# Kernel optimization log

Hardware: AMD Instinct MI355X
Metric: run time of the kernel (lower is better)

The kernel has to match this reference:

```python
import jax, jax.numpy as jnp
import numpy as np

D_MODEL = 96
N_HEAD = 3
HEAD_DIM = D_MODEL // N_HEAD  # 32
D_FF = 2048
WIDTH = 65
HALF_W = (WIDTH - 1) // 2  # 32
EPS = 1e-5


def layer_norm(x, g, b):
    mu = jnp.mean(x, axis=-1, keepdims=True)
    var = jnp.mean(jnp.square(x - mu), axis=-1, keepdims=True)
    return (x - mu) * jax.lax.rsqrt(var + EPS) * g + b


def setup_inputs() -> dict:
    key = jax.random.key(0)
    ks = jax.random.split(key, 8)
    B, T = 8, 2048
    s = 0.05
    return {
        "x": jax.random.normal(ks[0], (B, D_MODEL, T), dtype=jnp.float32),
        "w_qkv": jax.random.normal(ks[1], (3 * D_MODEL, D_MODEL), dtype=jnp.float32) * s,
        "b_qkv": jnp.zeros((3 * D_MODEL,), dtype=jnp.float32),
        "w_out": jax.random.normal(ks[2], (D_MODEL, D_MODEL), dtype=jnp.float32) * s,
        "b_out": jnp.zeros((D_MODEL,), dtype=jnp.float32),
        "ln1_g": jnp.ones((D_MODEL,), dtype=jnp.float32),
        "ln1_b": jnp.zeros((D_MODEL,), dtype=jnp.float32),
        "w_ff1": jax.random.normal(ks[3], (D_FF, D_MODEL), dtype=jnp.float32) * s,
        "b_ff1": jnp.zeros((D_FF,), dtype=jnp.float32),
        "w_ff2": jax.random.normal(ks[4], (D_MODEL, D_FF), dtype=jnp.float32) * s,
        "b_ff2": jnp.zeros((D_MODEL,), dtype=jnp.float32),
        "ln2_g": jnp.ones((D_MODEL,), dtype=jnp.float32),
        "ln2_b": jnp.zeros((D_MODEL,), dtype=jnp.float32),
        "lnf_g": jnp.ones((D_MODEL,), dtype=jnp.float32),
        "lnf_b": jnp.zeros((D_MODEL,), dtype=jnp.float32),
    }


def reference(x, w_qkv, b_qkv, w_out, b_out, ln1_g, ln1_b, w_ff1, b_ff1,
              w_ff2, b_ff2, ln2_g, ln2_b, lnf_g, lnf_b):
    # x: (B, C, T) -> (B, T, C)
    h = jnp.transpose(x, (0, 2, 1))
    B, T, C = h.shape

    # --- multi-head self-attention with banded mask ---
    qkv = h @ w_qkv.T + b_qkv                      # (B, T, 3C)
    q, k, v = jnp.split(qkv, 3, axis=-1)
    q = q.reshape(B, T, N_HEAD, HEAD_DIM)
    k = k.reshape(B, T, N_HEAD, HEAD_DIM)
    v = v.reshape(B, T, N_HEAD, HEAD_DIM)

    scale = 1.0 / jnp.sqrt(jnp.float32(HEAD_DIM))
    scores = jnp.einsum("bthd,bshd->bhts", q, k) * scale  # (B, H, T, T)

    idx = jnp.arange(T)
    band = jnp.abs(idx[:, None] - idx[None, :]) <= HALF_W  # |i-j| <= half width
    scores = jnp.where(band[None, None], scores, jnp.float32(-jnp.inf))

    attn = jax.nn.softmax(scores, axis=-1)
    ctx = jnp.einsum("bhts,bshd->bthd", attn, v).reshape(B, T, C)
    attn_out = ctx @ w_out.T + b_out

    # --- post-norm encoder layer (dropout inactive / eval mode) ---
    h = layer_norm(h + attn_out, ln1_g, ln1_b)
    ff = jax.nn.relu(h @ w_ff1.T + b_ff1) @ w_ff2.T + b_ff2
    h = layer_norm(h + ff, ln2_g, ln2_b)

    # extra layernorm applied when width is not None
    h = layer_norm(h, lnf_g, lnf_b)

    # (B, T, C) -> (B, C, T)
    return jnp.transpose(h, (0, 2, 1))
```

## Files before the change

### kernel.cpp

```cpp
#include <hip/hip_runtime.h>
#include <hip/hip_bf16.h>

#define B 8
#define T 2048
#define C 96
#define NH 3
#define HD 32
#define FFD 2048
#define HALF_W 32
#define BT (B*T)

typedef __hip_bfloat16 bf16;
typedef __attribute__((ext_vector_type(8))) short short8;
typedef __attribute__((ext_vector_type(4))) short short4v;
typedef __attribute__((ext_vector_type(16))) float floatx16;

__device__ __forceinline__ short f2bs(float v){
    __hip_bfloat16 h = __float2bfloat16(v);
    return *reinterpret_cast<short*>(&h);
}
__device__ __forceinline__ float bs2f(short s){
    unsigned u = ((unsigned)(unsigned short)s) << 16;
    return __uint_as_float(u);
}
__device__ __forceinline__ short8 ld_b64x2(const short* p){
    short4v a = *(const short4v*)p;
    short4v b = *(const short4v*)(p + 4);
    short8 v;
    v[0]=a[0]; v[1]=a[1]; v[2]=a[2]; v[3]=a[3];
    v[4]=b[0]; v[5]=b[1]; v[6]=b[2]; v[7]=b[3];
    return v;
}
__device__ __forceinline__ int4 exch_pair(int a0,int a1,int b0,int b1,int hq){
    int ra0=__shfl_xor(a0,32), ra1=__shfl_xor(a1,32);
    int rb0=__shfl_xor(b0,32), rb1=__shfl_xor(b1,32);
    int4 s;
    s.x = hq ? rb0 : a0;
    s.y = hq ? rb1 : a1;
    s.z = hq ? b0  : ra0;
    s.w = hq ? b1  : ra1;
    return s;
}
__device__ __forceinline__ void proj_pack(const floatx16& acc, const float* bias32, int hq,
                                          short8& f0, short8& f1){
    int pkq[4][2];
    #pragma unroll
    for(int q = 0; q < 4; ++q){
        float4 bv = *(const float4*)(bias32 + 8*q + 4*hq);
        short4v t;
        t[0]=f2bs(acc[4*q+0]+bv.x); t[1]=f2bs(acc[4*q+1]+bv.y);
        t[2]=f2bs(acc[4*q+2]+bv.z); t[3]=f2bs(acc[4*q+3]+bv.w);
        int2 u = *(int2*)&t; pkq[q][0]=u.x; pkq[q][1]=u.y;
    }
    int4 r0 = exch_pair(pkq[0][0],pkq[0][1],pkq[1][0],pkq[1][1],hq);
    int4 r1 = exch_pair(pkq[2][0],pkq[2][1],pkq[3][0],pkq[3][1],hq);
    f0 = *(short8*)&r0; f1 = *(short8*)&r1;
}

__global__ void cvtw_kernel(const float* __restrict__ wq, const float* __restrict__ wo,
                            const float* __restrict__ w1, const float* __restrict__ w2,
                            bf16* __restrict__ dst){
    int i = blockIdx.x*256 + threadIdx.x;
    if(i < 27648){
        int e = i&7, lane = (i>>3)&63, r = i>>9;
        int ks = r%6, ot = r/6;
        int o = ot*32 + (lane&31);
        int k = ks*16 + (lane>>5)*8 + e;
        dst[i] = __float2bfloat16(wq[o*96 + k]);
    } else if(i < 36864){
        int j = i - 27648;
        int e = j&7, lane = (j>>3)&63, r = j>>9;
        int ks = r%6, ct = r/6;
        int c = ct*32 + (lane&31);
        int k = ks*16 + (lane>>5)*8 + e;
        dst[i] = __float2bfloat16(wo[c*96 + k]);
    } else if(i < 233472){
        int j = i - 36864;
        int e = j&7, lane = (j>>3)&63, r = j>>9;
        int ks = r%6; r /= 6;
        int w = r%4, jt = r/4;
        int row = jt*128 + w*32 + (lane&31);
        int k = ks*16 + (lane>>5)*8 + e;
        dst[i] = __float2bfloat16(w1[row*96 + k]);
    } else if(i < 430080){
        int j = i - 233472;
        int e = j&7, lane = (j>>3)&63, r = j>>9;
        int ct = r%3; r /= 3;
        int g = r%2; r /= 2;
        int w = r%4, jt = r/4;
        int c = ct*32 + (lane&31);
        int k = jt*128 + w*32 + g*16 + (lane>>5)*8 + e;
        dst[i] = __float2bfloat16(w2[c*FFD + k]);
    }
}

__global__ __launch_bounds__(384, 4) void attn_kernel(
    const float* __restrict__ x,
    const bf16* __restrict__ wqs, const bf16* __restrict__ wos,
    const float* __restrict__ b_qkv, const float* __restrict__ b_out,
    const float* __restrict__ g1, const float* __restrict__ bb1,
    bf16* __restrict__ h1b){
    __shared__ __align__(16) char smem[45952];
    short* XS   = (short*)smem;
    short* PTS  = (short*)smem;
    short* VTS  = (short*)(smem + 19200);
    short* CTX  = (short*)(smem + 38400);
    float* LSS  = (float*)(smem + 44800);
    float* RED1 = (float*)(smem + 45184);

    const int tid = threadIdx.x;
    const int u = tid >> 6, lane = tid & 63;
    const int lm = lane & 31, hq = lane >> 5;
    const int grp = u / 3, h = u % 3;
    const int b  = blockIdx.x & 7;
    const int tt = blockIdx.x >> 3;
    const int t0 = tt * 32;
    const float* xb = x + (size_t)b*C*T;

    int tg0 = t0 - 32;
    if(tg0 >= 0 && t0 + 64 <= T){
        for(int e = tid; e < 96*24; e += 384){
            int c = e / 24, t4 = e % 24;
            float4 v = *(const float4*)(xb + (size_t)c*T + tg0 + t4*4);
            XS[(t4*4+0)*100 + c] = f2bs(v.x);
            XS[(t4*4+1)*100 + c] = f2bs(v.y);
            XS[(t4*4+2)*100 + c] = f2bs(v.z);
            XS[(t4*4+3)*100 + c] = f2bs(v.w);
        }
    } else {
        for(int e = tid; e < 96*96; e += 384){
            int c = e / 96, j = e % 96;
            int t = tg0 + j; t = t < 0 ? 0 : (t > T-1 ? T-1 : t);
            XS[j*100 + c] = f2bs(xb[(size_t)c*T + t]);
        }
    }
    __syncthreads();

    short8 wof[6];
    if(u < 3){
        #pragma unroll
        for(int ks = 0; ks < 6; ++ks)
            wof[ks] = *(const short8*)((const short*)wos + (size_t)(u*6 + ks)*512 + lane*8);
    }

    short8 kf[3][2], qf0, qf1;
    if(grp == 0){
        short8 kwf[6];
        #pragma unroll
        for(int ks = 0; ks < 6; ++ks)
            kwf[ks] = *(const short8*)((const short*)wqs + (size_t)((3+h)*6 + ks)*512 + lane*8);
        #pragma unroll
        for(int tau = 0; tau < 3; ++tau){
            short8 bfr[6];
            #pragma unroll
            for(int ks = 0; ks < 6; ++ks)
                bfr[ks] = *(const short8*)(XS + (tau*32+lm)*100 + ks*16 + hq*8);
            floatx16 acc;
            #pragma unroll
            for(int r = 0; r < 16; ++r) acc[r] = 0.f;
            #pragma unroll
            for(int ks = 0; ks < 6; ++ks)
                acc = __builtin_amdgcn_mfma_f32_32x32x16_bf16(kwf[ks], bfr[ks], acc, 0,0,0);
            proj_pack(acc, b_qkv + (3+h)*32, hq, kf[tau][0], kf[tau][1]);
            if(tau == 1){
                floatx16 qa;
                #pragma unroll
                for(int r = 0; r < 16; ++r) qa[r] = 0.f;
                #pragma unroll
                for(int ks = 0; ks < 6; ++ks){
                    short8 qwf = *(const short8*)((const short*)wqs + (size_t)(h*6 + ks)*512 + lane*8);
                    qa = __builtin_amdgcn_mfma_f32_32x32x16_bf16(qwf, bfr[ks], qa, 0,0,0);
                }
                proj_pack(qa, b_qkv + h*32, hq, qf0, qf1);
            }
        }
    } else {
        short8 vwf[6];
        #pragma unroll
        for(int ks = 0; ks < 6; ++ks)
            vwf[ks] = *(const short8*)((const short*)wqs + (size_t)((6+h)*6 + ks)*512 + lane*8);
        #pragma unroll
        for(int tau = 0; tau < 3; ++tau){
            short8 bfr[6];
            #pragma unroll
            for(int ks = 0; ks < 6; ++ks)
                bfr[ks] = *(const short8*)(XS + (tau*32+lm)*100 + ks*16 + hq*8);
            floatx16 acc;
            #pragma unroll
            for(int r = 0; r < 16; ++r) acc[r] = 0.f;
            #pragma unroll
            for(int ks = 0; ks < 6; ++ks)
                acc = __builtin_amdgcn_mfma_f32_32x32x16_bf16(vwf[ks], bfr[ks], acc, 0,0,0);
            #pragma unroll
            for(int q = 0; q < 4; ++q){
                float4 bv = *(const float4*)(b_qkv + (6+h)*32 + 8*q + 4*hq);
                float bva[4] = {bv.x, bv.y, bv.z, bv.w};
                #pragma unroll
                for(int r = 0; r < 4; ++r)
                    VTS[h*3200 + (8*q + 4*hq + r)*100 + tau*32 + lm] = f2bs(acc[4*q+r] + bva[r]);
            }
        }
    }
    __syncthreads();

    if(grp == 0){
        floatx16 S[3];
        #pragma unroll
        for(int sub = 0; sub < 3; ++sub){
            floatx16 z;
            #pragma unroll
            for(int r = 0; r < 16; ++r) z[r] = 0.f;
            z = __builtin_amdgcn_mfma_f32_32x32x16_bf16(kf[sub][0], qf0, z, 0,0,0);
            z = __builtin_amdgcn_mfma_f32_32x32x16_bf16(kf[sub][1], qf1, z, 0,0,0);
            S[sub] = z;
        }
        const float scale = 0.17677669529663687f;
        float part = 0.f;
        #pragma unroll
        for(int sub = 0; sub < 3; ++sub){
            #pragma unroll
            for(int r = 0; r < 16; ++r){
                int key_local = sub*32 + (r&3) + 8*(r>>2) + 4*hq;
                int s_glob = t0 - 32 + key_local;
                int rel = key_local - lm;
                bool ok = (rel >= 0) && (rel <= 64) && (s_glob >= 0) && (s_glob < T);
                float pe = ok ? __expf(S[sub][r]*scale) : 0.f;
                S[sub][r] = pe;
                part += pe;
            }
        }
        float ltot = part + __shfl_xor(part, 32);
        if(hq == 0) LSS[h*32 + lm] = ltot;
        #pragma unroll
        for(int sub = 0; sub < 3; ++sub){
            #pragma unroll
            for(int q4 = 0; q4 < 4; ++q4){
                int kbase = sub*32 + 8*q4 + 4*hq;
                short4v pk4;
                pk4[0] = f2bs(S[sub][4*q4+0]);
                pk4[1] = f2bs(S[sub][4*q4+1]);
                pk4[2] = f2bs(S[sub][4*q4+2]);
                pk4[3] = f2bs(S[sub][4*q4+3]);
                *(short4v*)(PTS + h*3200 + lm*100 + kbase) = pk4;
            }
        }
        floatx16 O;
        #pragma unroll
        for(int r = 0; r < 16; ++r) O[r] = 0.f;
        #pragma unroll
        for(int ks = 0; ks < 6; ++ks){
            short8 pa = ld_b64x2(PTS + h*3200 + lm*100 + ks*16 + hq*8);
            short8 vf = ld_b64x2(VTS + h*3200 + lm*100 + ks*16 + hq*8);
            O = __builtin_amdgcn_mfma_f32_32x32x16_bf16(pa, vf, O, 0,0,0);
        }
        #pragma unroll
        for(int r = 0; r < 16; ++r){
            int qr = (r&3) + 8*(r>>2) + 4*hq;
            float linv = 1.f / LSS[h*32 + qr];
            CTX[qr*100 + h*32 + lm] = f2bs(O[r]*linv);
        }
    }
    __syncthreads();

    float vals[16];
    if(u < 3){
        short8 cbfr[6];
        #pragma unroll
        for(int ks = 0; ks < 6; ++ks)
            cbfr[ks] = ld_b64x2(CTX + lm*100 + ks*16 + hq*8);
        floatx16 pacc;
        #pragma unroll
        for(int r = 0; r < 16; ++r) pacc[r] = 0.f;
        #pragma unroll
        for(int ks = 0; ks < 6; ++ks)
            pacc = __builtin_amdgcn_mfma_f32_32x32x16_bf16(wof[ks], cbfr[ks], pacc, 0,0,0);
        float p1 = 0.f, p2 = 0.f;
        #pragma unroll
        for(int q = 0; q < 4; ++q){
            int c = u*32 + 8*q + 4*hq;
            float4 bv = *(const float4*)(b_out + c);
            float bva[4] = {bv.x, bv.y, bv.z, bv.w};
            #pragma unroll
            for(int r = 0; r < 4; ++r){
                float xv = xb[(size_t)(c + r)*T + t0 + lm];
                float v = pacc[4*q+r] + bva[r] + xv;
                vals[4*q+r] = v;
                p1 += v; p2 += v*v;
            }
        }
        p1 += __shfl_xor(p1, 32);
        p2 += __shfl_xor(p2, 32);
        if(hq == 0){ RED1[u*32 + lm] = p1; RED1[96 + u*32 + lm] = p2; }
    }
    __syncthreads();
    if(u < 3){
        float s  = RED1[lm] + RED1[32 + lm] + RED1[64 + lm];
        float s2 = RED1[96 + lm] + RED1[128 + lm] + RED1[160 + lm];
        float mu = s * (1.0f/96.0f);
        float rstd = rsqrtf(s2*(1.0f/96.0f) - mu*mu + 1e-5f);
        int row = b*T + t0 + lm;
        #pragma unroll
        for(int q = 0; q < 4; ++q){
            int c = u*32 + 8*q + 4*hq;
            float4 gv = *(const float4*)(g1 + c);
            float4 bv = *(const float4*)(bb1 + c);
            float ga[4] = {gv.x, gv.y, gv.z, gv.w};
            float ba[4] = {bv.x, bv.y, bv.z, bv.w};
            short4v pkv;
            #pragma unroll
            for(int r = 0; r < 4; ++r)
                pkv[r] = f2bs((vals[4*q+r] - mu)*rstd*ga[r] + ba[r]);
            *(short4v*)((short*)h1b + (size_t)row*96 + c) = pkv;
        }
    }
}

__global__ __launch_bounds__(256, 2) void ff_kernel(
    const bf16* __restrict__ h1b,
    const bf16* __restrict__ w1s, const float* __restrict__ b1,
    const bf16* __restrict__ w2s, const float* __restrict__ b2,
    const float* __restrict__ g2, const float* __restrict__ bt2,
    const float* __restrict__ gf, const float* __restrict__ btf,
    float* __restrict__ out){
    __shared__ __align__(16) char smem[55296];
    float* REDP = (float*)smem;
    float* ZT   = (float*)smem;
    float* RED1 = (float*)(smem + 52224);
    float* RED2 = (float*)(smem + 53760);

    const int tid = threadIdx.x;
    const int w4 = tid >> 6, lane = tid & 63;
    const int lm = lane & 31, hq = lane >> 5;
    const int r0 = blockIdx.x * 64;
    const short* h1p = (const short*)h1b;

    short8 hf[2][6];
    #pragma unroll
    for(int mt = 0; mt < 2; ++mt)
        #pragma unroll
        for(int ks = 0; ks < 6; ++ks)
            hf[mt][ks] = *(const short8*)(h1p + (size_t)(r0 + mt*32 + lm)*96 + ks*16 + hq*8);

    floatx16 acc2[2][3];
    #pragma unroll
    for(int mt = 0; mt < 2; ++mt)
        #pragma unroll
        for(int i = 0; i < 3; ++i)
            #pragma unroll
            for(int r = 0; r < 16; ++r) acc2[mt][i][r] = 0.f;

    const short* w1b = (const short*)w1s + lane*8;
    const short* w2b = (const short*)w2s + lane*8;
    short8 cw1[6];
    #pragma unroll
    for(int ks = 0; ks < 6; ++ks)
        cw1[ks] = *(const short8*)(w1b + (size_t)(w4*6 + ks)*512);

    for(int it = 0; it < 16; ++it){
        const int J  = w4 + it*4;
        const int Jn = (it < 15) ? J + 4 : w4;
        short8 w2f[6];
        #pragma unroll
        for(int g = 0; g < 2; ++g)
            #pragma unroll
            for(int ct = 0; ct < 3; ++ct)
                w2f[g*3 + ct] = *(const short8*)(w2b + (size_t)((J*2 + g)*3 + ct)*512);
        short8 nw1[6];
        #pragma unroll
        for(int ks = 0; ks < 6; ++ks)
            nw1[ks] = *(const short8*)(w1b + (size_t)(Jn*6 + ks)*512);
        floatx16 a0, a1;
        #pragma unroll
        for(int r = 0; r < 16; ++r){ a0[r] = 0.f; a1[r] = 0.f; }
        #pragma unroll
        for(int ks = 0; ks < 6; ++ks){
            a0 = __builtin_amdgcn_mfma_f32_32x32x16_bf16(cw1[ks], hf[0][ks], a0, 0,0,0);
            a1 = __builtin_amdgcn_mfma_f32_32x32x16_bf16(cw1[ks], hf[1][ks], a1, 0,0,0);
        }
        int pk[2][4][2];
        #pragma unroll
        for(int q = 0; q < 4; ++q){
            float4 bv = *(const float4*)(b1 + J*32 + 8*q + 4*hq);
            float bva[4] = {bv.x, bv.y, bv.z, bv.w};
            short4v t0v, t1v;
            #pragma unroll
            for(int r = 0; r < 4; ++r){
                float v0 = a0[4*q+r] + bva[r];
                float v1 = a1[4*q+r] + bva[r];
                t0v[r] = f2bs(v0 > 0.f ? v0 : 0.f);
                t1v[r] = f2bs(v1 > 0.f ? v1 : 0.f);
            }
            int2 u0 = *(int2*)&t0v; int2 u1 = *(int2*)&t1v;
            pk[0][q][0] = u0.x; pk[0][q][1] = u0.y;
            pk[1][q][0] = u1.x; pk[1][q][1] = u1.y;
        }
        #pragma unroll
        for(int g = 0; g < 2; ++g){
            #pragma unroll
            for(int mt = 0; mt < 2; ++mt){
                int4 sfi = exch_pair(pk[mt][2*g][0], pk[mt][2*g][1],
                                     pk[mt][2*g+1][0], pk[mt][2*g+1][1], hq);
                short8 sf = *(short8*)&sfi;
                #pragma unroll
                for(int ct = 0; ct < 3; ++ct)
                    acc2[mt][ct] = __builtin_amdgcn_mfma_f32_32x32x16_bf16(
                                       w2f[g*3+ct], sf, acc2[mt][ct], 0,0,0);
            }
        }
        #pragma unroll
        for(int ks = 0; ks < 6; ++ks) cw1[ks] = nw1[ks];
    }

    float fv[2][16];
    float e1m[2], e2m[2];
    #pragma unroll
    for(int mt = 0; mt < 2; ++mt){
        #pragma unroll
        for(int ct = 0; ct < 3; ++ct)
            #pragma unroll
            for(int q = 0; q < 4; ++q)
                #pragma unroll
                for(int r = 0; r < 4; ++r)
                    REDP[(w4*3 + ct)*1088 + lane*17 + 4*q + r] = acc2[mt][ct][4*q+r];
        __syncthreads();
        if(w4 < 3){
            float e1 = 0.f, e2 = 0.f;
            #pragma unroll
            for(int q = 0; q < 4; ++q){
                int cb = w4*32 + 8*q + 4*hq;
                float4 bv = *(const float4*)(b2 + cb);
                float bva[4] = {bv.x, bv.y, bv.z, bv.w};
                short4v hv = *(const short4v*)(h1p + (size_t)(r0 + mt*32 + lm)*96 + cb);
                #pragma unroll
                for(int r = 0; r < 4; ++r){
                    float v = REDP[(0*3 + w4)*1088 + lane*17 + 4*q + r]
                            + REDP[(1*3 + w4)*1088 + lane*17 + 4*q + r]
                            + REDP[(2*3 + w4)*1088 + lane*17 + 4*q + r]
                            + REDP[(3*3 + w4)*1088 + lane*17 + 4*q + r]
                            + bva[r] + bs2f(hv[r]);
                    fv[mt][4*q+r] = v;
                    e1 += v; e2 += v*v;
                }
            }
            e1m[mt] = e1 + __shfl_xor(e1, 32);
            e2m[mt] = e2 + __shfl_xor(e2, 32);
        }
        __syncthreads();
    }
    if(w4 < 3 && hq == 0){
        #pragma unroll
        for(int mt = 0; mt < 2; ++mt){
            RED1[mt*192 + w4*32 + lm] = e1m[mt];
            RED1[mt*192 + 96 + w4*32 + lm] = e2m[mt];
        }
    }
    __syncthreads();
    float f1m[2], f2m[2];
    if(w4 < 3){
        #pragma unroll
        for(int mt = 0; mt < 2; ++mt){
            float s  = RED1[mt*192 + lm] + RED1[mt*192 + 32 + lm] + RED1[mt*192 + 64 + lm];
            float s2 = RED1[mt*192 + 96 + lm] + RED1[mt*192 + 128 + lm] + RED1[mt*192 + 160 + lm];
            float mu = s * (1.0f/96.0f);
            float rstd = rsqrtf(s2*(1.0f/96.0f) - mu*mu + 1e-5f);
            float f1 = 0.f, f2 = 0.f;
            #pragma unroll
            for(int q = 0; q < 4; ++q){
                int c = w4*32 + 8*q + 4*hq;
                float4 gv = *(const float4*)(g2 + c);
                float4 bv = *(const float4*)(bt2 + c);
                float ga[4] = {gv.x, gv.y, gv.z, gv.w};
                float ba[4] = {bv.x, bv.y, bv.z, bv.w};
                #pragma unroll
                for(int r = 0; r < 4; ++r){
                    float y = (fv[mt][4*q+r] - mu)*rstd*ga[r] + ba[r];
                    fv[mt][4*q+r] = y;
                    f1 += y; f2 += y*y;
                }
            }
            f1m[mt] = f1 + __shfl_xor(f1, 32);
            f2m[mt] = f2 + __shfl_xor(f2, 32);
        }
        if(hq == 0){
            #pragma unroll
            for(int mt = 0; mt < 2; ++mt){
                RED2[mt*192 + w4*32 + lm] = f1m[mt];
                RED2[mt*192 + 96 + w4*32 + lm] = f2m[mt];
            }
        }
    }
    __syncthreads();
    if(w4 < 3){
        #pragma unroll
        for(int mt = 0; mt < 2; ++mt){
            float s  = RED2[mt*192 + lm] + RED2[mt*192 + 32 + lm] + RED2[mt*192 + 64 + lm];
            float s2 = RED2[mt*192 + 96 + lm] + RED2[mt*192 + 128 + lm] + RED2[mt*192 + 160 + lm];
            float mu = s * (1.0f/96.0f);
            float rstd = rsqrtf(s2*(1.0f/96.0f) - mu*mu + 1e-5f);
            #pragma unroll
            for(int q = 0; q < 4; ++q){
                int c = w4*32 + 8*q + 4*hq;
                float4 gv = *(const float4*)(gf + c);
                float4 bv = *(const float4*)(btf + c);
                float ga[4] = {gv.x, gv.y, gv.z, gv.w};
                float ba[4] = {bv.x, bv.y, bv.z, bv.w};
                #pragma unroll
                for(int r = 0; r < 4; ++r)
                    ZT[(c + r)*68 + mt*32 + lm] = (fv[mt][4*q+r] - mu)*rstd*ga[r] + ba[r];
            }
        }
    }
    __syncthreads();
    const int bb = r0 / T, t0g = r0 % T;
    float* ob = out + (size_t)bb*C*T + t0g;
    for(int e = tid; e < 96*16; e += 256){
        int c = e >> 4, tg = e & 15;
        *(float4*)(ob + (size_t)c*T + tg*4) = *(const float4*)(ZT + c*68 + tg*4);
    }
}

extern "C" void kernel_launch(void* const* d_in, const int* in_sizes, int n_in,
                              void* d_out, int out_size, void* d_ws, size_t ws_size,
                              hipStream_t stream) {
    const float* x     = (const float*)d_in[0];
    const float* w_qkv = (const float*)d_in[1];
    const float* b_qkv = (const float*)d_in[2];
    const float* w_out = (const float*)d_in[3];
    const float* b_out = (const float*)d_in[4];
    const float* ln1_g = (const float*)d_in[5];
    const float* ln1_b = (const float*)d_in[6];
    const float* w_ff1 = (const float*)d_in[7];
    const float* b_ff1 = (const float*)d_in[8];
    const float* w_ff2 = (const float*)d_in[9];
    const float* b_ff2 = (const float*)d_in[10];
    const float* ln2_g = (const float*)d_in[11];
    const float* ln2_b = (const float*)d_in[12];
    const float* lnf_g = (const float*)d_in[13];
    const float* lnf_b = (const float*)d_in[14];
    float* out = (float*)d_out;

    char* wsb = (char*)d_ws;
    bf16* wts = (bf16*)wsb;
    bf16* wqs = wts;
    bf16* wos = wts + 27648;
    bf16* w1s = wts + 36864;
    bf16* w2s = wts + 233472;
    bf16* h1b = (bf16*)(wsb + 860160);

    cvtw_kernel<<<1680, 256, 0, stream>>>(w_qkv, w_out, w_ff1, w_ff2, wts);
    attn_kernel<<<512, 384, 0, stream>>>(x, wqs, wos, b_qkv, b_out,
                                         ln1_g, ln1_b, h1b);
    ff_kernel  <<<BT/64, 256, 0, stream>>>(h1b, w1s, b_ff1, w2s, b_ff2,
                                           ln2_g, ln2_b, lnf_g, lnf_b, out);
}
```

Baseline: 128.1 us.

## Fold weight conversion into attention kernel and drop separate conversion launch

```diff
diff --git a/kernel.cpp b/kernel.cpp
--- a/kernel.cpp
+++ b/kernel.cpp
@@ -29,6 +29,14 @@
     short8 v;
     v[0]=a[0]; v[1]=a[1]; v[2]=a[2]; v[3]=a[3];
     v[4]=b[0]; v[5]=b[1]; v[6]=b[2]; v[7]=b[3];
+    return v;
+}
+__device__ __forceinline__ short8 wfrag_f32(const float* wrow){
+    float4 a = *(const float4*)(wrow);
+    float4 b = *(const float4*)(wrow + 4);
+    short8 v;
+    v[0]=f2bs(a.x); v[1]=f2bs(a.y); v[2]=f2bs(a.z); v[3]=f2bs(a.w);
+    v[4]=f2bs(b.x); v[5]=f2bs(b.y); v[6]=f2bs(b.z); v[7]=f2bs(b.w);
     return v;
 }
 __device__ __forceinline__ int4 exch_pair(int a0,int a1,int b0,int b1,int hq){
@@ -57,48 +65,13 @@
     f0 = *(short8*)&r0; f1 = *(short8*)&r1;
 }
 
-__global__ void cvtw_kernel(const float* __restrict__ wq, const float* __restrict__ wo,
-                            const float* __restrict__ w1, const float* __restrict__ w2,
-                            bf16* __restrict__ dst){
-    int i = blockIdx.x*256 + threadIdx.x;
-    if(i < 27648){
-        int e = i&7, lane = (i>>3)&63, r = i>>9;
-        int ks = r%6, ot = r/6;
-        int o = ot*32 + (lane&31);
-        int k = ks*16 + (lane>>5)*8 + e;
-        dst[i] = __float2bfloat16(wq[o*96 + k]);
-    } else if(i < 36864){
-        int j = i - 27648;
-        int e = j&7, lane = (j>>3)&63, r = j>>9;
-        int ks = r%6, ct = r/6;
-        int c = ct*32 + (lane&31);
-        int k = ks*16 + (lane>>5)*8 + e;
-        dst[i] = __float2bfloat16(wo[c*96 + k]);
-    } else if(i < 233472){
-        int j = i - 36864;
-        int e = j&7, lane = (j>>3)&63, r = j>>9;
-        int ks = r%6; r /= 6;
-        int w = r%4, jt = r/4;
-        int row = jt*128 + w*32 + (lane&31);
-        int k = ks*16 + (lane>>5)*8 + e;
-        dst[i] = __float2bfloat16(w1[row*96 + k]);
-    } else if(i < 430080){
-        int j = i - 233472;
-        int e = j&7, lane = (j>>3)&63, r = j>>9;
-        int ct = r%3; r /= 3;
-        int g = r%2; r /= 2;
-        int w = r%4, jt = r/4;
-        int c = ct*32 + (lane&31);
-        int k = jt*128 + w*32 + g*16 + (lane>>5)*8 + e;
-        dst[i] = __float2bfloat16(w2[c*FFD + k]);
-    }
-}
-
 __global__ __launch_bounds__(384, 4) void attn_kernel(
     const float* __restrict__ x,
-    const bf16* __restrict__ wqs, const bf16* __restrict__ wos,
+    const float* __restrict__ wq, const float* __restrict__ wo,
+    const float* __restrict__ w1f, const float* __restrict__ w2f,
     const float* __restrict__ b_qkv, const float* __restrict__ b_out,
     const float* __restrict__ g1, const float* __restrict__ bb1,
+    bf16* __restrict__ w1s, bf16* __restrict__ w2s,
     bf16* __restrict__ h1b){
     __shared__ __align__(16) char smem[45952];
     short* XS   = (short*)smem;
@@ -116,6 +89,29 @@
     const int tt = blockIdx.x >> 3;
     const int t0 = tt * 32;
     const float* xb = x + (size_t)b*C*T;
+
+    {
+        const int base = blockIdx.x * 768;
+        #pragma unroll
+        for(int t2 = 0; t2 < 2; ++t2){
+            int j = base + tid + t2*384;
+            if(j < 196608){
+                int e = j&7, ln = (j>>3)&63, r = j>>9;
+                int ks = r%6, J = r/6;
+                int row = J*32 + (ln&31);
+                int k = ks*16 + (ln>>5)*8 + e;
+                w1s[j] = __float2bfloat16(w1f[row*96 + k]);
+            } else {
+                int jj = j - 196608;
+                int e = jj&7, ln = (jj>>3)&63, r = jj>>9;
+                int ct = r%3; r /= 3;
+                int g = r%2; int J = r/2;
+                int c = ct*32 + (ln&31);
+                int k = J*32 + g*16 + (ln>>5)*8 + e;
+                w2s[jj] = __float2bfloat16(w2f[c*FFD + k]);
+            }
+        }
+    }
 
     int tg0 = t0 - 32;
     if(tg0 >= 0 && t0 + 64 <= T){
@@ -140,7 +136,7 @@
     if(u < 3){
         #pragma unroll
         for(int ks = 0; ks < 6; ++ks)
-            wof[ks] = *(const short8*)((const short*)wos + (size_t)(u*6 + ks)*512 + lane*8);
+            wof[ks] = wfrag_f32(wo + (size_t)(u*32 + lm)*96 + ks*16 + hq*8);
     }
 
     short8 kf[3][2], qf0, qf1;
@@ -148,7 +144,7 @@
         short8 kwf[6];
         #pragma unroll
         for(int ks = 0; ks < 6; ++ks)
-            kwf[ks] = *(const short8*)((const short*)wqs + (size_t)((3+h)*6 + ks)*512 + lane*8);
+            kwf[ks] = wfrag_f32(wq + (size_t)((3+h)*32 + lm)*96 + ks*16 + hq*8);
         #pragma unroll
         for(int tau = 0; tau < 3; ++tau){
             short8 bfr[6];
@@ -168,7 +164,7 @@
                 for(int r = 0; r < 16; ++r) qa[r] = 0.f;
                 #pragma unroll
                 for(int ks = 0; ks < 6; ++ks){
-                    short8 qwf = *(const short8*)((const short*)wqs + (size_t)(h*6 + ks)*512 + lane*8);
+                    short8 qwf = wfrag_f32(wq + (size_t)(h*32 + lm)*96 + ks*16 + hq*8);
                     qa = __builtin_amdgcn_mfma_f32_32x32x16_bf16(qwf, bfr[ks], qa, 0,0,0);
                 }
                 proj_pack(qa, b_qkv + h*32, hq, qf0, qf1);
@@ -178,7 +174,7 @@
         short8 vwf[6];
         #pragma unroll
         for(int ks = 0; ks < 6; ++ks)
-            vwf[ks] = *(const short8*)((const short*)wqs + (size_t)((6+h)*6 + ks)*512 + lane*8);
+            vwf[ks] = wfrag_f32(wq + (size_t)((6+h)*32 + lm)*96 + ks*16 + hq*8);
         #pragma unroll
         for(int tau = 0; tau < 3; ++tau){
             short8 bfr[6];
@@ -540,16 +536,13 @@
     float* out = (float*)d_out;
 
     char* wsb = (char*)d_ws;
-    bf16* wts = (bf16*)wsb;
-    bf16* wqs = wts;
-    bf16* wos = wts + 27648;
-    bf16* w1s = wts + 36864;
-    bf16* w2s = wts + 233472;
-    bf16* h1b = (bf16*)(wsb + 860160);
-
-    cvtw_kernel<<<1680, 256, 0, stream>>>(w_qkv, w_out, w_ff1, w_ff2, wts);
-    attn_kernel<<<512, 384, 0, stream>>>(x, wqs, wos, b_qkv, b_out,
-                                         ln1_g, ln1_b, h1b);
+    bf16* w1s = (bf16*)wsb;
+    bf16* w2s = (bf16*)(wsb + 393216);
+    bf16* h1b = (bf16*)(wsb + 786432);
+
+    attn_kernel<<<512, 384, 0, stream>>>(x, w_qkv, w_out, w_ff1, w_ff2,
+                                         b_qkv, b_out, ln1_g, ln1_b,
+                                         w1s, w2s, h1b);
     ff_kernel  <<<BT/64, 256, 0, stream>>>(h1b, w1s, b_ff1, w2s, b_ff2,
                                            ln2_g, ln2_b, lnf_g, lnf_b, out);
 }
```

Result: slower. 138.6 us (+8.1%).
